# Kernel tuning notes

Hardware: AMD Instinct MI355X
Metric: run time of the kernel (lower is better)

The kernel has to match this reference:

```python
import jax, jax.numpy as jnp
import numpy as np

VOCAB, DIM, SEQ, DEPTH, WS, MULT = 32, 256, 8192, 6, 512, 4
BATCH = 2
NEG = -1e9  # mask fill value


def setup_inputs():
    key = jax.random.key(0)
    ks = jax.random.split(key, 8)
    L, d, h = DEPTH, DIM, DIM * MULT
    s = 0.02
    return {
        "tokens": jax.random.randint(ks[0], (BATCH, SEQ), 0, VOCAB),
        "embed": jax.random.normal(ks[1], (VOCAB, d)) * s,
        "ff_ln_s": jnp.ones((L, d)),
        "ff_ln_b": jnp.zeros((L, d)),
        "w1": jax.random.normal(ks[2], (L, d, h)) * s,
        "b1": jnp.zeros((L, h)),
        "w2": jax.random.normal(ks[3], (L, h, d)) * s,
        "b2": jnp.zeros((L, d)),
        "lnf_s": jnp.ones((d,)),
        "lnf_b": jnp.zeros((d,)),
        "w_out": jax.random.normal(ks[4], (d, VOCAB)) * s,
        "b_out": jnp.zeros((VOCAB,)),
    }


def layer_norm(x, s, b, eps=1e-5):
    m = jnp.mean(x, axis=-1, keepdims=True)
    v = jnp.var(x, axis=-1, keepdims=True)
    return (x - m) * jax.lax.rsqrt(v + eps) * s + b


def rotate_half(x):
    x1, x2 = jnp.split(x, 2, axis=-1)
    return jnp.concatenate([-x2, x1], axis=-1)


def local_attn(x, ws):
    # lucidrains LocalAttention: causal, look_backward=1, look_forward=0,
    # exact_windowsize=True, rotary pos emb on q/k. q = k = v = x (no projections).
    b, n, d = x.shape
    inv_freq = 1.0 / (10000.0 ** (jnp.arange(0, d, 2, dtype=jnp.float32) / d))
    t = jnp.arange(n, dtype=jnp.float32)
    fr = t[:, None] * inv_freq[None, :]
    fr = jnp.concatenate([fr, fr], axis=-1)  # (n, d)
    qk = x * jnp.cos(fr) + rotate_half(x) * jnp.sin(fr)  # rotary applied to q and k (identical)
    w = n // ws
    bq = qk.reshape(b, w, ws, d)
    bk = bq  # q == k here
    bv = x.reshape(b, w, ws, d)
    # look_around: each window sees [previous window, current window]
    pk = jnp.pad(bk, ((0, 0), (1, 0), (0, 0), (0, 0)))[:, :-1]
    pv = jnp.pad(bv, ((0, 0), (1, 0), (0, 0), (0, 0)))[:, :-1]
    bk2 = jnp.concatenate([pk, bk], axis=2)  # (b, w, 2*ws, d)
    bv2 = jnp.concatenate([pv, bv], axis=2)
    tq = jnp.arange(n).reshape(w, ws)
    tp = jnp.pad(tq, ((1, 0), (0, 0)), constant_values=-1)[:-1]
    tk = jnp.concatenate([tp, tq], axis=1)  # (w, 2*ws), -1 marks pad
    allowed = (
        (tk[:, None, :] >= 0)
        & (tq[:, :, None] >= tk[:, None, :])          # causal
        & (tq[:, :, None] <= tk[:, None, :] + ws)     # exact windowsize (look_backward=1)
    )
    sim = jnp.einsum("bwid,bwjd->bwij", bq, bk2) * (d ** -0.5)
    sim = jnp.where(allowed[None], sim, NEG)
    attn = jax.nn.softmax(sim, axis=-1)
    out = jnp.einsum("bwij,bwjd->bwid", attn, bv2)
    return out.reshape(b, n, d)


def reference(tokens, embed, ff_ln_s, ff_ln_b, w1, b1, w2, b2, lnf_s, lnf_b, w_out, b_out):
    x = embed[tokens]  # (b, n, d)
    for i in range(DEPTH):
        x = x + local_attn(x, WS)
        h = layer_norm(x, ff_ln_s[i], ff_ln_b[i])
        h = jax.nn.gelu(h @ w1[i] + b1[i], approximate=False)
        x = x + (h @ w2[i] + b2[i])
    return layer_norm(x, lnf_s, lnf_b) @ w_out + b_out  # (b, n, vocab)
```

## Files before the change

### kernel.cpp

```cpp
#include <hip/hip_runtime.h>
#include <hip/hip_bf16.h>
#include <math.h>

#define BATCH 2
#define SEQL 8192
#define DD 256
#define HDIM 1024
#define NLAYER 6
#define WSZ 512
#define NVOCAB 32
#define PLN (DD*HDIM)

typedef unsigned short u16;
typedef __attribute__((ext_vector_type(8))) short bf16x8;
typedef __attribute__((ext_vector_type(4))) float f32x4;

union B8 { uint4 u; bf16x8 b; ushort s[8]; uint w[4]; };

__device__ inline float bf2f(u16 v){
  unsigned int u = ((unsigned int)v) << 16;
  return __uint_as_float(u);
}
__device__ inline u16 f2bf(float f){
  unsigned int u = __float_as_uint(f);
  u += 0x7fff + ((u >> 16) & 1);
  return (u16)(u >> 16);
}
__device__ inline float4 bf4_to_f4(ushort4 v){
  return make_float4(bf2f(v.x), bf2f(v.y), bf2f(v.z), bf2f(v.w));
}

__global__ void k_tables(float* __restrict__ ct, float* __restrict__ st){
  int idx = blockIdx.x * 256 + threadIdx.x;
  if (idx >= SEQL * 128) return;
  int t = idx >> 7, i = idx & 127;
  double freq = exp(-((double)(2 * i) / (double)DD) * log(10000.0));
  double fr = (double)t * freq;
  ct[idx] = (float)cos(fr);
  st[idx] = (float)sin(fr);
}

__global__ void k_embed(const int* __restrict__ tokens, const float* __restrict__ emb,
                        float* __restrict__ x){
  int idx = blockIdx.x * 256 + threadIdx.x;
  int bt = idx >> 6, dv = (idx & 63) << 2;
  int tok = tokens[bt];
  *(float4*)(x + bt * DD + dv) = *(const float4*)(emb + tok * DD + dv);
}

__global__ void k_rope(const float* __restrict__ x, const float* __restrict__ ct,
                       const float* __restrict__ st, u16* __restrict__ qk,
                       u16* __restrict__ xv){
  int idx = blockIdx.x * 256 + threadIdx.x;
  int bt = idx >> 5, iv = (idx & 31) << 2;
  int t = bt & (SEQL - 1);
  const float* xr = x + bt * DD;
  float4 x1 = *(const float4*)(xr + iv);
  float4 x2 = *(const float4*)(xr + 128 + iv);
  float4 c = *(const float4*)(ct + t * 128 + iv);
  float4 s = *(const float4*)(st + t * 128 + iv);
  ushort4 q1, q2, v1, v2;
  q1.x = f2bf(x1.x * c.x - x2.x * s.x);  q2.x = f2bf(x2.x * c.x + x1.x * s.x);
  q1.y = f2bf(x1.y * c.y - x2.y * s.y);  q2.y = f2bf(x2.y * c.y + x1.y * s.y);
  q1.z = f2bf(x1.z * c.z - x2.z * s.z);  q2.z = f2bf(x2.z * c.z + x1.z * s.z);
  q1.w = f2bf(x1.w * c.w - x2.w * s.w);  q2.w = f2bf(x2.w * c.w + x1.w * s.w);
  v1.x = f2bf(x1.x); v1.y = f2bf(x1.y); v1.z = f2bf(x1.z); v1.w = f2bf(x1.w);
  v2.x = f2bf(x2.x); v2.y = f2bf(x2.y); v2.z = f2bf(x2.z); v2.w = f2bf(x2.w);
  *(ushort4*)(qk + bt * DD + iv)       = q1;
  *(ushort4*)(qk + bt * DD + 128 + iv) = q2;
  *(ushort4*)(xv + bt * DD + iv)       = v1;
  *(ushort4*)(xv + bt * DD + 128 + iv) = v2;
}

__global__ void __launch_bounds__(512, 2) k_attn2(const u16* __restrict__ qk,
                                                  const u16* __restrict__ xv,
                                                  const float* __restrict__ x,
                                                  float* __restrict__ y){
  __shared__ char smem[65536];
  u16* Klds = (u16*)smem;
  u16* Vlds = (u16*)(smem + 32768);
  float* redbuf = (float*)smem;

  const int tid = threadIdx.x;
  const int lane = tid & 63;
  const int w = tid >> 6;
  const int qh = w >> 1, kh = w & 1;
  const int l15 = lane & 15, lg = lane >> 4;

  const int qb = blockIdx.x * 64;
  const int t0 = qb & (SEQL - 1);
  const size_t bbase = (size_t)(qb >> 13) << 13;

  uint4 qf[8];
  {
    const u16* qr = qk + (size_t)(qb + qh*16 + l15) * DD + lg*4;
    #pragma unroll
    for (int s = 0; s < 8; ++s){
      uint2 a = *(const uint2*)(qr + s*32);
      uint2 b = *(const uint2*)(qr + s*32 + 16);
      qf[s] = make_uint4(a.x, a.y, b.x, b.y);
    }
  }

  f32x4 oacc[16];
  #pragma unroll
  for (int d = 0; d < 16; ++d) oacc[d] = (f32x4){0.f, 0.f, 0.f, 0.f};
  float lacc = 0.f;

  const int p0 = (t0 >= WSZ) ? (t0 - WSZ) : 0;
  const int ntile = ((t0 - p0) >> 6) + 1;

  const int sk15 = tid & 15, skt = (tid >> 4) & 3, sc = tid >> 6;
  const int sdh = tid & 31, sk0 = (tid >> 5) * 4;
  const int vkhw = sk0 >> 5, vh = (sk0 >> 4) & 1, vlgw = (sk0 >> 2) & 3;

  uint4 kreg[4];
  uint  vreg[4][4];

  {
    const u16* sb = qk + (bbase + (size_t)p0 + skt*16 + sk15) * DD;
    #pragma unroll
    for (int u = 0; u < 4; ++u) kreg[u] = *(const uint4*)(sb + u*64 + sc*8);
    #pragma unroll
    for (int u = 0; u < 4; ++u){
      int d0 = sdh*2 + u*64;
      const u16* vb = xv + (bbase + (size_t)p0 + sk0) * DD + d0;
      vreg[u][0] = *(const uint*)(vb);
      vreg[u][1] = *(const uint*)(vb + DD);
      vreg[u][2] = *(const uint*)(vb + 2*DD);
      vreg[u][3] = *(const uint*)(vb + 3*DD);
    }
  }
  #pragma unroll
  for (int u = 0; u < 4; ++u){
    int d0 = u*64 + sc*8;
    int s = d0 >> 5, r = d0 & 31;
    int h = r >> 4, lgw = (r & 15) >> 2;
    int rec = ((s*4 + skt)*4 + lgw)*16 + sk15;
    char* wp = (char*)Klds + rec*16 + h*8;
    *(uint2*)wp         = make_uint2(kreg[u].x, kreg[u].y);
    *(uint2*)(wp + 256) = make_uint2(kreg[u].z, kreg[u].w);
  }
  #pragma unroll
  for (int u = 0; u < 4; ++u){
    int d0 = sdh*2 + u*64;
    uint a0 = vreg[u][0], a1 = vreg[u][1], a2 = vreg[u][2], a3 = vreg[u][3];
    uint w0 = (a0 & 0xffffu) | (a1 << 16);
    uint w1 = (a2 & 0xffffu) | (a3 << 16);
    uint w2 = (a0 >> 16) | (a1 & 0xffff0000u);
    uint w3 = (a2 >> 16) | (a3 & 0xffff0000u);
    int dimt = d0 >> 4, d15 = d0 & 15;
    int rec = ((dimt*2 + vkhw)*4 + vlgw)*16 + d15;
    char* wp = (char*)Vlds + rec*16 + vh*8;
    *(uint2*)wp        = make_uint2(w0, w1);
    *(uint2*)(wp + 16) = make_uint2(w2, w3);
  }
  __syncthreads();

  for (int ti = 0; ti < ntile; ++ti){
    const int p = p0 + ti*64;
    if (ti + 1 < ntile){
      const int pn = p + 64;
      const u16* sb = qk + (bbase + (size_t)pn + skt*16 + sk15) * DD;
      #pragma unroll
      for (int u = 0; u < 4; ++u) kreg[u] = *(const uint4*)(sb + u*64 + sc*8);
      #pragma unroll
      for (int u = 0; u < 4; ++u){
        int d0 = sdh*2 + u*64;
        const u16* vb = xv + (bbase + (size_t)pn + sk0) * DD + d0;
        vreg[u][0] = *(const uint*)(vb);
        vreg[u][1] = *(const uint*)(vb + DD);
        vreg[u][2] = *(const uint*)(vb + 2*DD);
        vreg[u][3] = *(const uint*)(vb + 3*DD);
      }
    }

    f32x4 sacc[2];
    sacc[0] = (f32x4){0.f,0.f,0.f,0.f};
    sacc[1] = (f32x4){0.f,0.f,0.f,0.f};
    #pragma unroll
    for (int s = 0; s < 8; ++s){
      B8 ka0, ka1, qbf;
      ka0.b = *(const bf16x8*)((char*)Klds + (((s*4 + kh*2+0)*4 + lg)*16 + l15)*16);
      ka1.b = *(const bf16x8*)((char*)Klds + (((s*4 + kh*2+1)*4 + lg)*16 + l15)*16);
      qbf.u = qf[s];
      sacc[0] = __builtin_amdgcn_mfma_f32_16x16x32_bf16(ka0.b, qbf.b, sacc[0], 0, 0, 0);
      sacc[1] = __builtin_amdgcn_mfma_f32_16x16x32_bf16(ka1.b, qbf.b, sacc[1], 0, 0, 0);
    }

    B8 pa;
    #pragma unroll
    for (int ktp = 0; ktp < 2; ++ktp){
      int kbase = p + kh*32 + ktp*16 + lg*4;
      int qpos = t0 + qh*16 + l15;
      #pragma unroll
      for (int r = 0; r < 4; ++r){
        int kpos = kbase + r;
        float sv = sacc[ktp][r] * 0.0625f;
        bool ok = (kpos <= qpos) && (qpos <= kpos + WSZ);
        float pv = ok ? __expf(sv) : 0.0f;
        lacc += pv;
        pa.s[ktp*4 + r] = f2bf(pv);
      }
    }

    #pragma unroll
    for (int dimt = 0; dimt < 16; ++dimt){
      B8 vb;
      vb.b = *(const bf16x8*)((char*)Vlds + (((dimt*2 + kh)*4 + lg)*16 + l15)*16);
      oacc[dimt] = __builtin_amdgcn_mfma_f32_16x16x32_bf16(pa.b, vb.b, oacc[dimt], 0, 0, 0);
    }

    __syncthreads();
    if (ti + 1 < ntile){
      #pragma unroll
      for (int u = 0; u < 4; ++u){
        int d0 = u*64 + sc*8;
        int s = d0 >> 5, r = d0 & 31;
        int h = r >> 4, lgw = (r & 15) >> 2;
        int rec = ((s*4 + skt)*4 + lgw)*16 + sk15;
        char* wp = (char*)Klds + rec*16 + h*8;
        *(uint2*)wp         = make_uint2(kreg[u].x, kreg[u].y);
        *(uint2*)(wp + 256) = make_uint2(kreg[u].z, kreg[u].w);
      }
      #pragma unroll
      for (int u = 0; u < 4; ++u){
        int d0 = sdh*2 + u*64;
        uint a0 = vreg[u][0], a1 = vreg[u][1], a2 = vreg[u][2], a3 = vreg[u][3];
        uint w0 = (a0 & 0xffffu) | (a1 << 16);
        uint w1 = (a2 & 0xffffu) | (a3 << 16);
        uint w2 = (a0 >> 16) | (a1 & 0xffff0000u);
        uint w3 = (a2 >> 16) | (a3 & 0xffff0000u);
        int dimt = d0 >> 4, d15 = d0 & 15;
        int rec = ((dimt*2 + vkhw)*4 + vlgw)*16 + d15;
        char* wp = (char*)Vlds + rec*16 + vh*8;
        *(uint2*)wp        = make_uint2(w0, w1);
        *(uint2*)(wp + 16) = make_uint2(w2, w3);
      }
    }
    __syncthreads();
  }

  lacc += __shfl_xor(lacc, 16, 64);
  lacc += __shfl_xor(lacc, 32, 64);
  if (lane < 16) redbuf[kh*64 + qh*16 + l15] = lacc;
  __syncthreads();
  if (tid < 64) redbuf[128 + tid] = redbuf[tid] + redbuf[64 + tid];
  __syncthreads();

  float* opass = redbuf + 192;
  #pragma unroll
  for (int pass = 0; pass < 8; ++pass){
    #pragma unroll
    for (int dt = 0; dt < 2; ++dt){
      int dimt = pass*2 + dt;
      #pragma unroll
      for (int r = 0; r < 4; ++r){
        int qrow = qh*16 + lg*4 + r;
        opass[(kh*64 + qrow)*36 + dt*16 + l15] = oacc[dimt][r];
      }
    }
    __syncthreads();
    {
      int q = tid >> 3, dv = (tid & 7) * 4;
      float4 o0 = *(float4*)&opass[q*36 + dv];
      float4 o1 = *(float4*)&opass[(64 + q)*36 + dv];
      float inv = 1.0f / redbuf[128 + q];
      size_t gi = (size_t)(qb + q) * DD + pass*32 + dv;
      float4 xr = *(const float4*)(x + gi);
      float4 ov;
      ov.x = xr.x + (o0.x + o1.x) * inv;
      ov.y = xr.y + (o0.y + o1.y) * inv;
      ov.z = xr.z + (o0.z + o1.z) * inv;
      ov.w = xr.w + (o0.w + o1.w) * inv;
      *(float4*)(y + gi) = ov;
    }
    __syncthreads();
  }
}

__global__ void __launch_bounds__(256) k_ln(const float* __restrict__ in,
                                            const float* __restrict__ g,
                                            const float* __restrict__ b,
                                            u16* __restrict__ out){
  int wid = (blockIdx.x * 256 + threadIdx.x) >> 6;
  int lane = threadIdx.x & 63;
  float4 v = *(const float4*)(in + wid * DD + lane * 4);
  float s = v.x + v.y + v.z + v.w;
  float ss = v.x * v.x + v.y * v.y + v.z * v.z + v.w * v.w;
  #pragma unroll
  for (int o = 32; o; o >>= 1){ s += __shfl_xor(s, o, 64); ss += __shfl_xor(ss, o, 64); }
  float m = s * (1.0f / DD);
  float var = ss * (1.0f / DD) - m * m;
  float rs = rsqrtf(var + 1e-5f);
  float4 gf = *(const float4*)(g + lane * 4);
  float4 bf = *(const float4*)(b + lane * 4);
  ushort4 o4;
  o4.x = f2bf((v.x - m) * rs * gf.x + bf.x);
  o4.y = f2bf((v.y - m) * rs * gf.y + bf.y);
  o4.z = f2bf((v.z - m) * rs * gf.z + bf.z);
  o4.w = f2bf((v.w - m) * rs * gf.w + bf.w);
  *(ushort4*)(out + wid * DD + lane * 4) = o4;
}

template<int KDIM, int NDIM>
__device__ __forceinline__ void split_one(const float* __restrict__ W,
                                          u16* __restrict__ Phi,
                                          u16* __restrict__ Plo, int idx){
  int c15 = idx & 15;
  int lg = (idx >> 4) & 3;
  int nt = (idx >> 6) % (NDIM/16);
  int ks = idx / ((NDIM/16) * 64);
  int col = nt*16 + c15;
  B8 hi, lo;
  #pragma unroll
  for (int j = 0; j < 8; ++j){
    int k = ks*32 + (j >> 2)*16 + lg*4 + (j & 3);
    float wv = W[(size_t)k * NDIM + col];
    u16 hv = f2bf(wv);
    hi.s[j] = hv;
    lo.s[j] = f2bf(wv - bf2f(hv));
  }
  *(uint4*)(Phi + (size_t)idx * 8) = hi.u;
  *(uint4*)(Plo + (size_t)idx * 8) = lo.u;
}

__global__ void __launch_bounds__(256) k_split2(const float* __restrict__ W1,
                                                const float* __restrict__ W2,
                                                u16* __restrict__ P){
  int b = blockIdx.x;
  if (b < 128) split_one<DD, HDIM>(W1, P, P + PLN, b*256 + threadIdx.x);
  else         split_one<HDIM, DD>(W2, P + 2*PLN, P + 3*PLN, (b - 128)*256 + threadIdx.x);
}

template<int KDIM, int NDIM, int EPI>
__global__ void __launch_bounds__(256) k_gemm(const u16* __restrict__ A,
                                              const u16* __restrict__ BhG,
                                              const u16* __restrict__ BlG,
                                              const float* __restrict__ bias,
                                              const float* __restrict__ res,
                                              float* __restrict__ outf,
                                              u16* __restrict__ outh){
  __shared__ char smem[51200];
  char* As = smem;
  char* Bh = smem + 18432;
  char* Bl = smem + 34816;

  const int tid = threadIdx.x;
  const int lane = tid & 63;
  const int w = tid >> 6;
  const int wr = w >> 1, wc = w & 1;
  const int l15 = lane & 15, lg = lane >> 4;
  const int m0 = blockIdx.y * 128;
  const int n0 = blockIdx.x * 128;

  f32x4 acc[4][4];
  #pragma unroll
  for (int a = 0; a < 4; ++a)
    #pragma unroll
    for (int c = 0; c < 4; ++c)
      acc[a][c] = (f32x4){0.f,0.f,0.f,0.f};

  for (int kb = 0; kb < KDIM/64; ++kb){
    __syncthreads();
    #pragma unroll
    for (int p = 0; p < 4; ++p){
      int c = p*256 + tid;
      int row = c >> 3, cc = c & 7;
      uint4 v = *(const uint4*)(A + (size_t)(m0 + row) * KDIM + kb*64 + cc*8);
      *(uint4*)(As + row*144 + cc*16) = v;
    }
    #pragma unroll
    for (int s = 0; s < 2; ++s){
      size_t gbase = ((size_t)(kb*2 + s) * (NDIM/16) + (n0 >> 4)) * 64;
      const uint4* srcH = (const uint4*)BhG + gbase;
      const uint4* srcL = (const uint4*)BlG + gbase;
      #pragma unroll
      for (int rr = 0; rr < 2; ++rr){
        int r = rr*256 + tid;
        *(uint4*)(Bh + (s*512 + r)*16) = srcH[r];
        *(uint4*)(Bl + (s*512 + r)*16) = srcL[r];
      }
    }
    __syncthreads();

    #pragma unroll
    for (int s = 0; s < 2; ++s){
      B8 af[4], bhf[4], blf[4];
      #pragma unroll
      for (int a = 0; a < 4; ++a){
        const char* ab = As + (wr*64 + a*16 + l15)*144 + s*64 + lg*8;
        uint2 lo = *(const uint2*)ab;
        uint2 hi = *(const uint2*)(ab + 32);
        af[a].u = make_uint4(lo.x, lo.y, hi.x, hi.y);
      }
      #pragma unroll
      for (int c = 0; c < 4; ++c){
        int rec = s*512 + (wc*4 + c)*64 + lg*16 + l15;
        bhf[c].u = *(const uint4*)(Bh + rec*16);
        blf[c].u = *(const uint4*)(Bl + rec*16);
      }
      #pragma unroll
      for (int a = 0; a < 4; ++a)
        #pragma unroll
        for (int c = 0; c < 4; ++c){
          acc[a][c] = __builtin_amdgcn_mfma_f32_16x16x32_bf16(af[a].b, bhf[c].b, acc[a][c], 0, 0, 0);
          acc[a][c] = __builtin_amdgcn_mfma_f32_16x16x32_bf16(af[a].b, blf[c].b, acc[a][c], 0, 0, 0);
        }
    }
  }

  float bv[4];
  #pragma unroll
  for (int c = 0; c < 4; ++c) bv[c] = bias[n0 + wc*64 + c*16 + l15];

  #pragma unroll
  for (int a = 0; a < 4; ++a){
    #pragma unroll
    for (int c = 0; c < 4; ++c){
      #pragma unroll
      for (int r = 0; r < 4; ++r){
        int row = m0 + wr*64 + a*16 + lg*4 + r;
        int col = n0 + wc*64 + c*16 + l15;
        float v = acc[a][c][r] + bv[c];
        if (EPI == 0){
          float gl = 0.5f * v * (1.0f + erff(v * 0.70710678f));
          outh[(size_t)row * NDIM + col] = f2bf(gl);
        } else {
          outf[(size_t)row * NDIM + col] = v + res[(size_t)row * NDIM + col];
        }
      }
    }
  }
}

__global__ void __launch_bounds__(256) k_final(const float* __restrict__ x,
                                               const float* __restrict__ g,
                                               const float* __restrict__ b,
                                               const float* __restrict__ wout,
                                               const float* __restrict__ bout,
                                               float* __restrict__ out){
  __shared__ float lds[4][256];
  int widx = threadIdx.x >> 6, lane = threadIdx.x & 63;
  int bt = blockIdx.x * 4 + widx;
  float4 v = *(const float4*)(x + bt * DD + lane * 4);
  float s = v.x + v.y + v.z + v.w;
  float ss = v.x * v.x + v.y * v.y + v.z * v.z + v.w * v.w;
  #pragma unroll
  for (int o = 32; o; o >>= 1){ s += __shfl_xor(s, o, 64); ss += __shfl_xor(ss, o, 64); }
  float m = s * (1.0f / DD);
  float var = ss * (1.0f / DD) - m * m;
  float rs = rsqrtf(var + 1e-5f);
  float4 gf = *(const float4*)(g + lane * 4);
  float4 bf = *(const float4*)(b + lane * 4);
  lds[widx][lane * 4 + 0] = (v.x - m) * rs * gf.x + bf.x;
  lds[widx][lane * 4 + 1] = (v.y - m) * rs * gf.y + bf.y;
  lds[widx][lane * 4 + 2] = (v.z - m) * rs * gf.z + bf.z;
  lds[widx][lane * 4 + 3] = (v.w - m) * rs * gf.w + bf.w;
  __syncthreads();
  int vo = lane & 31, half = lane >> 5;
  const float* lp = &lds[widx][half * 128];
  const float* wp = wout + half * 128 * NVOCAB + vo;
  float acc = 0;
  #pragma unroll 4
  for (int d = 0; d < 128; ++d) acc += lp[d] * wp[d * NVOCAB];
  acc += __shfl_down(acc, 32, 64);
  if (lane < 32) out[bt * NVOCAB + vo] = acc + bout[vo];
}

extern "C" void kernel_launch(void* const* d_in, const int* in_sizes, int n_in,
                              void* d_out, int out_size, void* d_ws, size_t ws_size,
                              hipStream_t stream) {
  const int*   tokens = (const int*)d_in[0];
  const float* emb   = (const float*)d_in[1];
  const float* ffs   = (const float*)d_in[2];
  const float* ffb   = (const float*)d_in[3];
  const float* w1    = (const float*)d_in[4];
  const float* b1    = (const float*)d_in[5];
  const float* w2    = (const float*)d_in[6];
  const float* b2    = (const float*)d_in[7];
  const float* lnfs  = (const float*)d_in[8];
  const float* lnfb  = (const float*)d_in[9];
  const float* wout  = (const float*)d_in[10];
  const float* bout  = (const float*)d_in[11];
  float* out = (float*)d_out;

  char* ws = (char*)d_ws;
  float* x    = (float*)(ws);
  float* y    = (float*)(ws + (size_t)16*1024*1024);
  u16*   buf8 = (u16*)  (ws + (size_t)32*1024*1024);
  u16*   qk   = (u16*)  (ws + (size_t)40*1024*1024);
  u16*   h    = (u16*)  (ws + (size_t)48*1024*1024);
  float* ct   = (float*)(ws + (size_t)80*1024*1024);
  float* st   = (float*)(ws + (size_t)84*1024*1024);

  k_tables<<<4096, 256, 0, stream>>>(ct, st);
  k_embed<<<4096, 256, 0, stream>>>(tokens, emb, x);
  for (int L = 0; L < NLAYER; ++L){
    k_rope<<<2048, 256, 0, stream>>>(x, ct, st, qk, buf8);
    k_attn2<<<256, 512, 0, stream>>>(qk, buf8, x, y);
    k_ln  <<<4096, 256, 0, stream>>>(y, ffs + L*DD, ffb + L*DD, buf8);
    k_split2<<<256, 256, 0, stream>>>(w1 + (size_t)L*PLN, w2 + (size_t)L*PLN, qk);
    k_gemm<DD, HDIM, 0><<<dim3(8, 128), 256, 0, stream>>>(
        buf8, qk, qk + PLN, b1 + L*HDIM, nullptr, nullptr, h);
    k_gemm<HDIM, DD, 1><<<dim3(2, 128), 256, 0, stream>>>(
        h, qk + 2*PLN, qk + 3*PLN, b2 + L*DD, y, x, nullptr);
  }
  k_final<<<4096, 256, 0, stream>>>(x, lnfs, lnfb, wout, bout, out);
}
```

Before: 804.9 us.

## Halve attention and GEMM block tiles, use direct global-to-LDS loads

The attention kernel moves from 512-thread blocks over 64 queries to 256-thread blocks over 32 queries, so each thread stages twice as much K/V. The FFN GEMMs halve the N tile to 64 with a merged B buffer filled by global_load_lds, and launch twice as many blocks. The rope table kernel switches from double to float math. The aim is more blocks in flight and less LDS and register pressure. The cost is more redundant K/V and A-tile traffic across blocks, and some rope-table precision.

```diff
diff --git a/kernel.cpp b/kernel.cpp
--- a/kernel.cpp
+++ b/kernel.cpp
@@ -26,18 +26,21 @@
   u += 0x7fff + ((u >> 16) & 1);
   return (u16)(u >> 16);
 }
-__device__ inline float4 bf4_to_f4(ushort4 v){
-  return make_float4(bf2f(v.x), bf2f(v.y), bf2f(v.z), bf2f(v.w));
+
+__device__ __forceinline__ void gload16(const void* g, void* l){
+  __builtin_amdgcn_global_load_lds(
+      (const __attribute__((address_space(1))) unsigned int*)g,
+      (__attribute__((address_space(3))) unsigned int*)l, 16, 0, 0);
 }
 
 __global__ void k_tables(float* __restrict__ ct, float* __restrict__ st){
   int idx = blockIdx.x * 256 + threadIdx.x;
   if (idx >= SEQL * 128) return;
   int t = idx >> 7, i = idx & 127;
-  double freq = exp(-((double)(2 * i) / (double)DD) * log(10000.0));
-  double fr = (double)t * freq;
-  ct[idx] = (float)cos(fr);
-  st[idx] = (float)sin(fr);
+  float freq = expf(-((float)i / 128.0f) * 9.210340371976184f);
+  float fr = (float)t * freq;
+  ct[idx] = cosf(fr);
+  st[idx] = sinf(fr);
 }
 
 __global__ void k_embed(const int* __restrict__ tokens, const float* __restrict__ emb,
@@ -72,7 +75,7 @@
   *(ushort4*)(xv + bt * DD + 128 + iv) = v2;
 }
 
-__global__ void __launch_bounds__(512, 2) k_attn2(const u16* __restrict__ qk,
+__global__ void __launch_bounds__(256, 2) k_attn2(const u16* __restrict__ qk,
                                                   const u16* __restrict__ xv,
                                                   const float* __restrict__ x,
                                                   float* __restrict__ y){
@@ -87,7 +90,7 @@
   const int qh = w >> 1, kh = w & 1;
   const int l15 = lane & 15, lg = lane >> 4;
 
-  const int qb = blockIdx.x * 64;
+  const int qb = blockIdx.x * 32;
   const int t0 = qb & (SEQL - 1);
   const size_t bbase = (size_t)(qb >> 13) << 13;
 
@@ -111,29 +114,32 @@
   const int ntile = ((t0 - p0) >> 6) + 1;
 
   const int sk15 = tid & 15, skt = (tid >> 4) & 3, sc = tid >> 6;
-  const int sdh = tid & 31, sk0 = (tid >> 5) * 4;
-  const int vkhw = sk0 >> 5, vh = (sk0 >> 4) & 1, vlgw = (sk0 >> 2) & 3;
-
-  uint4 kreg[4];
-  uint  vreg[4][4];
+  const int sdh = tid & 31, skg = tid >> 5;
+
+  uint4 kreg[8];
+  uint  vreg[2][4][4];
 
   {
     const u16* sb = qk + (bbase + (size_t)p0 + skt*16 + sk15) * DD;
     #pragma unroll
-    for (int u = 0; u < 4; ++u) kreg[u] = *(const uint4*)(sb + u*64 + sc*8);
-    #pragma unroll
-    for (int u = 0; u < 4; ++u){
-      int d0 = sdh*2 + u*64;
-      const u16* vb = xv + (bbase + (size_t)p0 + sk0) * DD + d0;
-      vreg[u][0] = *(const uint*)(vb);
-      vreg[u][1] = *(const uint*)(vb + DD);
-      vreg[u][2] = *(const uint*)(vb + 2*DD);
-      vreg[u][3] = *(const uint*)(vb + 3*DD);
-    }
-  }
-  #pragma unroll
-  for (int u = 0; u < 4; ++u){
-    int d0 = u*64 + sc*8;
+    for (int u = 0; u < 8; ++u) kreg[u] = *(const uint4*)(sb + u*32 + sc*8);
+    #pragma unroll
+    for (int kg = 0; kg < 2; ++kg){
+      int sk0 = (skg + kg*8) * 4;
+      #pragma unroll
+      for (int u = 0; u < 4; ++u){
+        int d0 = sdh*2 + u*64;
+        const u16* vb = xv + (bbase + (size_t)p0 + sk0) * DD + d0;
+        vreg[kg][u][0] = *(const uint*)(vb);
+        vreg[kg][u][1] = *(const uint*)(vb + DD);
+        vreg[kg][u][2] = *(const uint*)(vb + 2*DD);
+        vreg[kg][u][3] = *(const uint*)(vb + 3*DD);
+      }
+    }
+  }
+  #pragma unroll
+  for (int u = 0; u < 8; ++u){
+    int d0 = u*32 + sc*8;
     int s = d0 >> 5, r = d0 & 31;
     int h = r >> 4, lgw = (r & 15) >> 2;
     int rec = ((s*4 + skt)*4 + lgw)*16 + sk15;
@@ -142,18 +148,23 @@
     *(uint2*)(wp + 256) = make_uint2(kreg[u].z, kreg[u].w);
   }
   #pragma unroll
-  for (int u = 0; u < 4; ++u){
-    int d0 = sdh*2 + u*64;
-    uint a0 = vreg[u][0], a1 = vreg[u][1], a2 = vreg[u][2], a3 = vreg[u][3];
-    uint w0 = (a0 & 0xffffu) | (a1 << 16);
-    uint w1 = (a2 & 0xffffu) | (a3 << 16);
-    uint w2 = (a0 >> 16) | (a1 & 0xffff0000u);
-    uint w3 = (a2 >> 16) | (a3 & 0xffff0000u);
-    int dimt = d0 >> 4, d15 = d0 & 15;
-    int rec = ((dimt*2 + vkhw)*4 + vlgw)*16 + d15;
-    char* wp = (char*)Vlds + rec*16 + vh*8;
-    *(uint2*)wp        = make_uint2(w0, w1);
-    *(uint2*)(wp + 16) = make_uint2(w2, w3);
+  for (int kg = 0; kg < 2; ++kg){
+    int sk0 = (skg + kg*8) * 4;
+    int vkhw = sk0 >> 5, vh = (sk0 >> 4) & 1, vlgw = (sk0 >> 2) & 3;
+    #pragma unroll
+    for (int u = 0; u < 4; ++u){
+      int d0 = sdh*2 + u*64;
+      uint a0 = vreg[kg][u][0], a1 = vreg[kg][u][1], a2 = vreg[kg][u][2], a3 = vreg[kg][u][3];
+      uint w0 = (a0 & 0xffffu) | (a1 << 16);
+      uint w1 = (a2 & 0xffffu) | (a3 << 16);
+      uint w2 = (a0 >> 16) | (a1 & 0xffff0000u);
+      uint w3 = (a2 >> 16) | (a3 & 0xffff0000u);
+      int dimt = d0 >> 4, d15 = d0 & 15;
+      int rec = ((dimt*2 + vkhw)*4 + vlgw)*16 + d15;
+      char* wp = (char*)Vlds + rec*16 + vh*8;
+      *(uint2*)wp        = make_uint2(w0, w1);
+      *(uint2*)(wp + 16) = make_uint2(w2, w3);
+    }
   }
   __syncthreads();
 
@@ -163,15 +174,19 @@
       const int pn = p + 64;
       const u16* sb = qk + (bbase + (size_t)pn + skt*16 + sk15) * DD;
       #pragma unroll
-      for (int u = 0; u < 4; ++u) kreg[u] = *(const uint4*)(sb + u*64 + sc*8);
-      #pragma unroll
-      for (int u = 0; u < 4; ++u){
-        int d0 = sdh*2 + u*64;
-        const u16* vb = xv + (bbase + (size_t)pn + sk0) * DD + d0;
-        vreg[u][0] = *(const uint*)(vb);
-        vreg[u][1] = *(const uint*)(vb + DD);
-        vreg[u][2] = *(const uint*)(vb + 2*DD);
-        vreg[u][3] = *(const uint*)(vb + 3*DD);
+      for (int u = 0; u < 8; ++u) kreg[u] = *(const uint4*)(sb + u*32 + sc*8);
+      #pragma unroll
+      for (int kg = 0; kg < 2; ++kg){
+        int sk0 = (skg + kg*8) * 4;
+        #pragma unroll
+        for (int u = 0; u < 4; ++u){
+          int d0 = sdh*2 + u*64;
+          const u16* vb = xv + (bbase + (size_t)pn + sk0) * DD + d0;
+          vreg[kg][u][0] = *(const uint*)(vb);
+          vreg[kg][u][1] = *(const uint*)(vb + DD);
+          vreg[kg][u][2] = *(const uint*)(vb + 2*DD);
+          vreg[kg][u][3] = *(const uint*)(vb + 3*DD);
+        }
       }
     }
 
@@ -214,8 +229,8 @@
     __syncthreads();
     if (ti + 1 < ntile){
       #pragma unroll
-      for (int u = 0; u < 4; ++u){
-        int d0 = u*64 + sc*8;
+      for (int u = 0; u < 8; ++u){
+        int d0 = u*32 + sc*8;
         int s = d0 >> 5, r = d0 & 31;
         int h = r >> 4, lgw = (r & 15) >> 2;
         int rec = ((s*4 + skt)*4 + lgw)*16 + sk15;
@@ -224,18 +239,23 @@
         *(uint2*)(wp + 256) = make_uint2(kreg[u].z, kreg[u].w);
       }
       #pragma unroll
-      for (int u = 0; u < 4; ++u){
-        int d0 = sdh*2 + u*64;
-        uint a0 = vreg[u][0], a1 = vreg[u][1], a2 = vreg[u][2], a3 = vreg[u][3];
-        uint w0 = (a0 & 0xffffu) | (a1 << 16);
-        uint w1 = (a2 & 0xffffu) | (a3 << 16);
-        uint w2 = (a0 >> 16) | (a1 & 0xffff0000u);
-        uint w3 = (a2 >> 16) | (a3 & 0xffff0000u);
-        int dimt = d0 >> 4, d15 = d0 & 15;
-        int rec = ((dimt*2 + vkhw)*4 + vlgw)*16 + d15;
-        char* wp = (char*)Vlds + rec*16 + vh*8;
-        *(uint2*)wp        = make_uint2(w0, w1);
-        *(uint2*)(wp + 16) = make_uint2(w2, w3);
+      for (int kg = 0; kg < 2; ++kg){
+        int sk0 = (skg + kg*8) * 4;
+        int vkhw = sk0 >> 5, vh = (sk0 >> 4) & 1, vlgw = (sk0 >> 2) & 3;
+        #pragma unroll
+        for (int u = 0; u < 4; ++u){
+          int d0 = sdh*2 + u*64;
+          uint a0 = vreg[kg][u][0], a1 = vreg[kg][u][1], a2 = vreg[kg][u][2], a3 = vreg[kg][u][3];
+          uint w0 = (a0 & 0xffffu) | (a1 << 16);
+          uint w1 = (a2 & 0xffffu) | (a3 << 16);
+          uint w2 = (a0 >> 16) | (a1 & 0xffff0000u);
+          uint w3 = (a2 >> 16) | (a3 & 0xffff0000u);
+          int dimt = d0 >> 4, d15 = d0 & 15;
+          int rec = ((dimt*2 + vkhw)*4 + vlgw)*16 + d15;
+          char* wp = (char*)Vlds + rec*16 + vh*8;
+          *(uint2*)wp        = make_uint2(w0, w1);
+          *(uint2*)(wp + 16) = make_uint2(w2, w3);
+        }
       }
     }
     __syncthreads();
@@ -243,12 +263,12 @@
 
   lacc += __shfl_xor(lacc, 16, 64);
   lacc += __shfl_xor(lacc, 32, 64);
-  if (lane < 16) redbuf[kh*64 + qh*16 + l15] = lacc;
+  if (lane < 16) redbuf[kh*32 + qh*16 + l15] = lacc;
   __syncthreads();
-  if (tid < 64) redbuf[128 + tid] = redbuf[tid] + redbuf[64 + tid];
+  if (tid < 32) redbuf[64 + tid] = redbuf[tid] + redbuf[32 + tid];
   __syncthreads();
 
-  float* opass = redbuf + 192;
+  float* opass = redbuf + 96;
   #pragma unroll
   for (int pass = 0; pass < 8; ++pass){
     #pragma unroll
@@ -257,15 +277,15 @@
       #pragma unroll
       for (int r = 0; r < 4; ++r){
         int qrow = qh*16 + lg*4 + r;
-        opass[(kh*64 + qrow)*36 + dt*16 + l15] = oacc[dimt][r];
+        opass[(kh*32 + qrow)*36 + dt*16 + l15] = oacc[dimt][r];
       }
     }
     __syncthreads();
     {
       int q = tid >> 3, dv = (tid & 7) * 4;
       float4 o0 = *(float4*)&opass[q*36 + dv];
-      float4 o1 = *(float4*)&opass[(64 + q)*36 + dv];
-      float inv = 1.0f / redbuf[128 + q];
+      float4 o1 = *(float4*)&opass[(32 + q)*36 + dv];
+      float inv = 1.0f / redbuf[64 + q];
       size_t gi = (size_t)(qb + q) * DD + pass*32 + dv;
       float4 xr = *(const float4*)(x + gi);
       float4 ov;
@@ -341,10 +361,9 @@
                                               const float* __restrict__ res,
                                               float* __restrict__ outf,
                                               u16* __restrict__ outh){
-  __shared__ char smem[51200];
+  __shared__ char smem[18432 + 16384];
   char* As = smem;
-  char* Bh = smem + 18432;
-  char* Bl = smem + 34816;
+  char* Bs = smem + 18432;
 
   const int tid = threadIdx.x;
   const int lane = tid & 63;
@@ -352,14 +371,15 @@
   const int wr = w >> 1, wc = w & 1;
   const int l15 = lane & 15, lg = lane >> 4;
   const int m0 = blockIdx.y * 128;
-  const int n0 = blockIdx.x * 128;
-
-  f32x4 acc[4][4];
-  #pragma unroll
-  for (int a = 0; a < 4; ++a)
-    #pragma unroll
-    for (int c = 0; c < 4; ++c)
-      acc[a][c] = (f32x4){0.f,0.f,0.f,0.f};
+  const int n0 = blockIdx.x * 64;
+  const int NT16 = NDIM / 16;
+
+  f32x4 acc[4][2];
+  #pragma unroll
+  for (int a = 0; a < 4; ++a){
+    acc[a][0] = (f32x4){0.f,0.f,0.f,0.f};
+    acc[a][1] = (f32x4){0.f,0.f,0.f,0.f};
+  }
 
   for (int kb = 0; kb < KDIM/64; ++kb){
     __syncthreads();
@@ -371,22 +391,19 @@
       *(uint4*)(As + row*144 + cc*16) = v;
     }
     #pragma unroll
+    for (int p = 0; p < 4; ++p){
+      int j = p*256 + tid;
+      int plane = j >> 9, rem = j & 511;
+      int chunk = rem >> 6, r = rem & 63;
+      const u16* src = (plane ? BlG : BhG)
+          + (((size_t)(kb*2 + (chunk >> 2)) * NT16 + (n0 >> 4) + (chunk & 3))*64 + r)*8;
+      gload16(src, Bs + j*16);
+    }
+    __syncthreads();
+
+    #pragma unroll
     for (int s = 0; s < 2; ++s){
-      size_t gbase = ((size_t)(kb*2 + s) * (NDIM/16) + (n0 >> 4)) * 64;
-      const uint4* srcH = (const uint4*)BhG + gbase;
-      const uint4* srcL = (const uint4*)BlG + gbase;
-      #pragma unroll
-      for (int rr = 0; rr < 2; ++rr){
-        int r = rr*256 + tid;
-        *(uint4*)(Bh + (s*512 + r)*16) = srcH[r];
-        *(uint4*)(Bl + (s*512 + r)*16) = srcL[r];
-      }
-    }
-    __syncthreads();
-
-    #pragma unroll
-    for (int s = 0; s < 2; ++s){
-      B8 af[4], bhf[4], blf[4];
+      B8 af[4], bhf[2], blf[2];
       #pragma unroll
       for (int a = 0; a < 4; ++a){
         const char* ab = As + (wr*64 + a*16 + l15)*144 + s*64 + lg*8;
@@ -395,33 +412,33 @@
         af[a].u = make_uint4(lo.x, lo.y, hi.x, hi.y);
       }
       #pragma unroll
-      for (int c = 0; c < 4; ++c){
-        int rec = s*512 + (wc*4 + c)*64 + lg*16 + l15;
-        bhf[c].u = *(const uint4*)(Bh + rec*16);
-        blf[c].u = *(const uint4*)(Bl + rec*16);
+      for (int c = 0; c < 2; ++c){
+        int off = (((s*4 + wc*2 + c)*64) + lg*16 + l15)*16;
+        bhf[c].u = *(const uint4*)(Bs + off);
+        blf[c].u = *(const uint4*)(Bs + 8192 + off);
       }
       #pragma unroll
       for (int a = 0; a < 4; ++a)
         #pragma unroll
-        for (int c = 0; c < 4; ++c){
+        for (int c = 0; c < 2; ++c){
           acc[a][c] = __builtin_amdgcn_mfma_f32_16x16x32_bf16(af[a].b, bhf[c].b, acc[a][c], 0, 0, 0);
           acc[a][c] = __builtin_amdgcn_mfma_f32_16x16x32_bf16(af[a].b, blf[c].b, acc[a][c], 0, 0, 0);
         }
     }
   }
 
-  float bv[4];
-  #pragma unroll
-  for (int c = 0; c < 4; ++c) bv[c] = bias[n0 + wc*64 + c*16 + l15];
+  float bv[2];
+  bv[0] = bias[n0 + wc*32 + l15];
+  bv[1] = bias[n0 + wc*32 + 16 + l15];
 
   #pragma unroll
   for (int a = 0; a < 4; ++a){
     #pragma unroll
-    for (int c = 0; c < 4; ++c){
+    for (int c = 0; c < 2; ++c){
       #pragma unroll
       for (int r = 0; r < 4; ++r){
         int row = m0 + wr*64 + a*16 + lg*4 + r;
-        int col = n0 + wc*64 + c*16 + l15;
+        int col = n0 + wc*32 + c*16 + l15;
         float v = acc[a][c][r] + bv[c];
         if (EPI == 0){
           float gl = 0.5f * v * (1.0f + erff(v * 0.70710678f));
@@ -498,12 +515,12 @@
   k_embed<<<4096, 256, 0, stream>>>(tokens, emb, x);
   for (int L = 0; L < NLAYER; ++L){
     k_rope<<<2048, 256, 0, stream>>>(x, ct, st, qk, buf8);
-    k_attn2<<<256, 512, 0, stream>>>(qk, buf8, x, y);
+    k_attn2<<<512, 256, 0, stream>>>(qk, buf8, x, y);
     k_ln  <<<4096, 256, 0, stream>>>(y, ffs + L*DD, ffb + L*DD, buf8);
     k_split2<<<256, 256, 0, stream>>>(w1 + (size_t)L*PLN, w2 + (size_t)L*PLN, qk);
-    k_gemm<DD, HDIM, 0><<<dim3(8, 128), 256, 0, stream>>>(
+    k_gemm<DD, HDIM, 0><<<dim3(16, 128), 256, 0, stream>>>(
         buf8, qk, qk + PLN, b1 + L*HDIM, nullptr, nullptr, h);
-    k_gemm<HDIM, DD, 1><<<dim3(2, 128), 256, 0, stream>>>(
+    k_gemm<HDIM, DD, 1><<<dim3(4, 128), 256, 0, stream>>>(
         h, qk + 2*PLN, qk + 3*PLN, b2 + L*DD, y, x, nullptr);
   }
   k_final<<<4096, 256, 0, stream>>>(x, lnfs, lnfb, wout, bout, out);
```

Measured after the change: 817.4 us. About the same (+1.6%).
